# Kernel tuning notes

Measured on AMD Instinct MI355X. Metric: run time of the kernel, lower is better.

Reference implementation:

```python
import jax, jax.numpy as jnp
import numpy as np

B, W, D = 8, 1024, 1024
HEADS, KDIM, VDIM = 16, 64, 64


def setup_inputs() -> dict:
    key = jax.random.key(0)
    k1, k2, k3, k4 = jax.random.split(key, 4)
    # he_normal-ish scaling for weights
    s = (2.0 / D) ** 0.5
    return {
        "inputs": jax.random.normal(k1, (B, W, D), dtype=jnp.float32),
        "Wq": jax.random.normal(k2, (D, HEADS * KDIM), dtype=jnp.float32) * s,
        "Wk": jax.random.normal(k3, (D, HEADS * KDIM), dtype=jnp.float32) * s,
        "Wv": jax.random.normal(k4, (D, HEADS * VDIM), dtype=jnp.float32) * s,
    }


def reference(inputs, Wq, Wk, Wv):
    # Self-attention: memory = inputs
    bsz, win, _ = inputs.shape
    # DenseHeads: linear projection, reshaped to (B, W, heads, head_units)
    q = (inputs @ Wq).reshape(bsz, win, HEADS, KDIM)
    k = (inputs @ Wk).reshape(bsz, win, HEADS, KDIM)
    v = (inputs @ Wv).reshape(bsz, win, HEADS, VDIM)
    scale = KDIM ** (-0.5)
    # scores[b,q,h,m] = sum_k Q[b,q,h,k] * K[b,m,h,k]
    scores = jnp.einsum("bqhk,bmhk->bqhm", q, k) * scale
    attn = jax.nn.softmax(scores, axis=-1)
    # out[b,q,h,v] = sum_m attn[b,q,h,m] * V[b,m,h,v]
    out = jnp.einsum("bqhm,bmhv->bqhv", attn, v)
    return out
```

## Files before the change

### kernel.cpp

```cpp
#include <hip/hip_runtime.h>
#include <stdint.h>


using bf16x8 = __attribute__((ext_vector_type(8))) __bf16;
using f32x4  = __attribute__((ext_vector_type(4))) float;
using f16x4  = __attribute__((ext_vector_type(4))) _Float16;

union frag_u  { uint4 u4; bf16x8 f; };
union vfrag_u { uint2 u2; f16x4 f; };
union pfrag_u { unsigned int u[2]; f16x4 f; };

__device__ inline unsigned short f2bf(float x){
  unsigned int u = __float_as_uint(x);
  u += 0x7fffu + ((u >> 16) & 1u);
  return (unsigned short)(u >> 16);
}

__device__ inline unsigned int pkrtz_u32(float a, float b){
  auto r = __builtin_amdgcn_cvt_pkrtz(a, b);
  unsigned int u; __builtin_memcpy(&u, &r, 4); return u;
}

__device__ inline void gl_lds16(const void* g, void* l){
  __builtin_amdgcn_global_load_lds(
      (const __attribute__((address_space(1))) void*)g,
      (__attribute__((address_space(3))) void*)l, 16, 0, 0);
}

#define SBAR() do{ asm volatile("" ::: "memory"); __builtin_amdgcn_s_barrier(); asm volatile("" ::: "memory"); }while(0)
#define VMC(n)  asm volatile("s_waitcnt vmcnt(" #n ")" ::: "memory")

__global__ void cast_all(const float* __restrict__ X,
                         const float* __restrict__ Wq, const float* __restrict__ Wk,
                         const float* __restrict__ Wv,
                         unsigned short* __restrict__ Xb,
                         unsigned short* __restrict__ Wt){
  __shared__ float tile[64][65];
  int bid = blockIdx.x;
  if (bid < 8192){
    int i = (bid * 256 + threadIdx.x) * 4;
    float4 v = *(const float4*)(X + i);
    ushort4 o;
    o.x = f2bf(v.x); o.y = f2bf(v.y); o.z = f2bf(v.z); o.w = f2bf(v.w);
    *(ushort4*)(Xb + i) = o;
    return;
  }
  int id = bid - 8192;
  int proj = id >> 8;
  int rem  = id & 255;
  int kt = rem & 15, nt = rem >> 4;
  const float* Wsrc = (proj == 0) ? Wq : ((proj == 1) ? Wk : Wv);
  int k0 = kt * 64, n0 = nt * 64;
  int tx = threadIdx.x & 63, ty = threadIdx.x >> 6;
  for (int i = 0; i < 16; i++){
    int k = i * 4 + ty;
    tile[k][tx] = Wsrc[(k0 + k) * 1024 + n0 + tx];
  }
  __syncthreads();
  for (int i = 0; i < 16; i++){
    int n = i * 4 + ty;
    Wt[(proj * 1024 + n0 + n) * 1024 + k0 + tx] = f2bf(tile[tx][n]);
  }
}

__global__ __launch_bounds__(512, 2) void gemm_qkv(
    const unsigned short* __restrict__ Xb,
    const unsigned short* __restrict__ Wt,
    unsigned short* __restrict__ QK,
    unsigned short* __restrict__ Vt){
  __shared__ __align__(16) char Abuf[2][32768];
  __shared__ __align__(16) char Bbuf[2][24576];

  int bid = blockIdx.x;
  int tau = (bid & 7) * 64 + (bid >> 3);
  int by = tau >> 4, bx = tau & 15;
  int tid = threadIdx.x;
  int w = tid >> 6, lane = tid & 63;
  int li = lane & 15, g = lane >> 4;
  int lrow = lane >> 3;
  int wr = w >> 2, wc = w & 3;

  int xcol = ((lane & 7) ^ lrow) << 3;
  int aoff[4], boff[3];
#pragma unroll
  for (int j = 0; j < 4; j++)
    aoff[j] = (by * 256 + (j * 8 + w) * 8 + lrow) * 1024 + xcol;
#pragma unroll
  for (int j = 0; j < 3; j++)
    boff[j] = (bx * 192 + (j * 8 + w) * 8 + lrow) * 1024 + xcol;

  int swz  = (li & 7) << 4;
  int colA0 = (g * 16) ^ swz;
  int colA1 = (64 + g * 16) ^ swz;
  int aBase = (wr * 128 + li) * 128;
  int bBase = (wc * 48 + li) * 128;

  f32x4 acc[8][3] = {};
  frag_u bfr[3][2], a0[2][2], a1[2][2];

#define STA(buf, j, tt) gl_lds16(Xb + aoff[j] + (tt) * 64, &Abuf[buf][((j) * 8 + w) * 1024])
#define STB(buf, j, tt) gl_lds16(Wt + boff[j] + (tt) * 64, &Bbuf[buf][((j) * 8 + w) * 1024])
#define LDA(S, buf, m0) do{ \
  S[0][0].u4 = *(const uint4*)&Abuf[buf][aBase + (m0)     * 2048 + colA0]; \
  S[0][1].u4 = *(const uint4*)&Abuf[buf][aBase + (m0)     * 2048 + colA1]; \
  S[1][0].u4 = *(const uint4*)&Abuf[buf][aBase + (m0 + 1) * 2048 + colA0]; \
  S[1][1].u4 = *(const uint4*)&Abuf[buf][aBase + (m0 + 1) * 2048 + colA1]; }while(0)
#define LDB(buf) do{ \
  _Pragma("unroll") for (int n = 0; n < 3; n++){ \
    bfr[n][0].u4 = *(const uint4*)&Bbuf[buf][bBase + n * 2048 + colA0]; \
    bfr[n][1].u4 = *(const uint4*)&Bbuf[buf][bBase + n * 2048 + colA1]; } }while(0)
#define MFMAP(S, P) do{ __builtin_amdgcn_s_setprio(1); \
  _Pragma("unroll") for (int kk = 0; kk < 2; kk++) \
  _Pragma("unroll") for (int i = 0; i < 2; i++) \
  _Pragma("unroll") for (int n = 0; n < 3; n++) \
    acc[(P) * 2 + i][n] = __builtin_amdgcn_mfma_f32_16x16x32_bf16( \
        S[i][kk].f, bfr[n][kk].f, acc[(P) * 2 + i][n], 0, 0, 0); \
  __builtin_amdgcn_s_setprio(0); }while(0)

  STB(0, 0, 0); STB(0, 1, 0); STB(0, 2, 0);
  STA(0, 0, 0); STA(0, 1, 0); STA(0, 2, 0); STA(0, 3, 0);
  STB(1, 0, 1); STB(1, 1, 1); STB(1, 2, 1);
  VMC(3);
  SBAR();

  for (int t = 0; t < 16; ++t){
    int cur = t & 1, nxt = cur ^ 1;
    LDB(cur); LDA(a0, cur, 0);
    LDA(a1, cur, 2);
    if (t < 15){ STA(nxt, 0, t + 1); STA(nxt, 1, t + 1); }
    SBAR();
    MFMAP(a0, 0);
    SBAR();
    LDA(a0, cur, 4);
    if (t < 15){ STA(nxt, 2, t + 1); STA(nxt, 3, t + 1); }
    SBAR();
    MFMAP(a1, 1);
    SBAR();
    LDA(a1, cur, 6);
    if (t < 14){ STB(cur, 0, t + 2); STB(cur, 1, t + 2); }
    SBAR();
    MFMAP(a0, 2);
    SBAR();
    if (t < 14) STB(cur, 2, t + 2);
    SBAR();
    MFMAP(a1, 3);
    if (t < 14) { VMC(3); }
    else if (t == 14) { VMC(0); }
    SBAR();
  }
#undef STA
#undef STB
#undef LDA
#undef LDB
#undef MFMAP

  int row0 = by * 256 + wr * 128 + g * 4;
  int bb16 = (by >> 2) * 16;
#pragma unroll
  for (int n = 0; n < 3; n++){
    int cb = bx * 192 + wc * 48 + n * 16;
    if (cb < 2048){
      float sc = (cb < 1024) ? 0.1803368801111f : 1.0f;
#pragma unroll
      for (int m = 0; m < 8; m++){
        int row = row0 + m * 16;
#pragma unroll
        for (int r = 0; r < 4; r++)
          QK[(size_t)(row + r) * 2048 + cb + li] = f2bf(acc[m][n][r] * sc);
      }
    } else {
      int vc = cb + li - 2048;
      int hh = vc >> 6, dd = vc & 63;
#pragma unroll
      for (int m = 0; m < 8; m++){
        int mtok = (row0 + m * 16) & 1023;
        uint2 cv;
        cv.x = pkrtz_u32(acc[m][n][0], acc[m][n][1]);
        cv.y = pkrtz_u32(acc[m][n][2], acc[m][n][3]);
        *(uint2*)(Vt + ((size_t)(bb16 + hh) * 64 + dd) * 1024 + mtok) = cv;
      }
    }
  }
}

__global__ __launch_bounds__(256, 4) void attn(const unsigned short* __restrict__ QK,
                                               const unsigned short* __restrict__ Vt,
                                               float* __restrict__ Out){
  __shared__ __align__(16) unsigned short Kbuf[64 * 64];
  __shared__ __align__(16) unsigned short Vbuf[64 * 64];
  int id = blockIdx.x;
  int bh = id & 127, qb = id >> 7;
  int b = bh >> 4, h = bh & 15;
  int w = threadIdx.x >> 6, lane = threadIdx.x & 63;
  int g = lane >> 4, li = lane & 15;
  int lrow = lane >> 3, lcol = lane & 7;
  int scol = ((lcol ^ lrow) & 7) * 8;

  frag_u qf[2];
  {
    int tok = b * 1024 + qb * 64 + w * 16 + li;
    const unsigned short* qp = QK + (size_t)tok * 2048 + h * 64 + g * 8;
    qf[0].u4 = *(const uint4*)(qp);
    qf[1].u4 = *(const uint4*)(qp + 32);
  }

  f32x4 o[4] = {};
  f32x4 osum = {};
  const f32x4 bias = {-10.f, -10.f, -10.f, -10.f};
  pfrag_u ones;
  ones.u[0] = 0x3c003c00u; ones.u[1] = 0x3c003c00u;

  const unsigned short* Kg = QK + (size_t)b * 1024 * 2048 + 1024 + h * 64;
  const unsigned short* Vg = Vt + (size_t)bh * 65536;

  for (int mt = 0; mt < 16; mt++){
    int m0 = mt * 64;
    __syncthreads();
    for (int i = 0; i < 2; i++){
      int idx = w * 2 + i;
      int row = idx * 8 + lrow;
      gl_lds16(Kg + (size_t)(m0 + row) * 2048 + scol, Kbuf + idx * 512);
      gl_lds16(Vg + row * 1024 + m0 + scol,           Vbuf + idx * 512);
    }
    __syncthreads();

    f32x4 s[4];
    for (int t = 0; t < 4; t++) s[t] = bias;
    for (int t = 0; t < 4; t++){
      for (int c = 0; c < 2; c++){
        frag_u kf;
        kf.u4 = *(const uint4*)(Kbuf + (t * 16 + li) * 64 + ((((c << 2) + g) ^ (li & 7)) << 3));
        s[t] = __builtin_amdgcn_mfma_f32_16x16x32_bf16(kf.f, qf[c].f, s[t], 0, 0, 0);
      }
    }

    pfrag_u pf[4];
    for (int t = 0; t < 4; t++){
      float p0 = __builtin_exp2f(s[t][0]);
      float p1 = __builtin_exp2f(s[t][1]);
      float p2 = __builtin_exp2f(s[t][2]);
      float p3 = __builtin_exp2f(s[t][3]);
      pf[t].u[0] = pkrtz_u32(p0, p1);
      pf[t].u[1] = pkrtz_u32(p2, p3);
    }

    for (int t = 0; t < 4; t++)
      osum = __builtin_amdgcn_mfma_f32_16x16x16f16(ones.f, pf[t].f, osum, 0, 0, 0);
    for (int tv = 0; tv < 4; tv++){
      for (int t = 0; t < 4; t++){
        int gg = ((t * 2 + (g >> 1)) ^ (li & 7));
        vfrag_u vf;
        vf.u2 = *(const uint2*)(Vbuf + (tv * 16 + li) * 64 + gg * 8 + (g & 1) * 4);
        o[tv] = __builtin_amdgcn_mfma_f32_16x16x16f16(vf.f, pf[t].f, o[tv], 0, 0, 0);
      }
    }
  }

  float inv = 1.f / osum[0];

  int tok = b * 1024 + qb * 64 + w * 16 + li;
  float* op = Out + (size_t)tok * 1024 + h * 64 + g * 4;
  for (int tv = 0; tv < 4; tv++){
    float4 v4;
    v4.x = o[tv][0] * inv; v4.y = o[tv][1] * inv;
    v4.z = o[tv][2] * inv; v4.w = o[tv][3] * inv;
    *(float4*)(op + tv * 16) = v4;
  }
}

extern "C" void kernel_launch(void* const* d_in, const int* in_sizes, int n_in,
                              void* d_out, int out_size, void* d_ws, size_t ws_size,
                              hipStream_t stream) {
  const float* X  = (const float*)d_in[0];
  const float* Wq = (const float*)d_in[1];
  const float* Wk = (const float*)d_in[2];
  const float* Wv = (const float*)d_in[3];
  float* Out = (float*)d_out;
  char* ws = (char*)d_ws;
  unsigned short* Xb = (unsigned short*)(ws);
  unsigned short* Wt = (unsigned short*)(ws + (size_t)16 * 1024 * 1024);
  unsigned short* QK = (unsigned short*)(ws + (size_t)22 * 1024 * 1024);
  unsigned short* Vt = (unsigned short*)(ws + (size_t)54 * 1024 * 1024);

  cast_all<<<8960, 256, 0, stream>>>(X, Wq, Wk, Wv, Xb, Wt);
  gemm_qkv<<<512, 512, 0, stream>>>(Xb, Wt, QK, Vt);
  attn    <<<2048, 256, 0, stream>>>(QK, Vt, Out);
}
```

Measured before the change: 214.1 us.

## Split QKV GEMM tile across 16 waves with fewer accumulators per wave

Doubles the gemm_qkv block to 1024 threads (16 waves), so each wave computes a 64x48 sub-tile instead of 128x48. This halves the accumulator registers per wave and cuts the number of barriers per k-step. The global-to-LDS loads are redistributed so 8 waves issue two B loads and the rest issue one. More waves per block add latency hiding, but the larger workgroup brings heavier barrier synchronisation and less register headroom per wave.

```diff
diff --git a/kernel.cpp b/kernel.cpp
--- a/kernel.cpp
+++ b/kernel.cpp
@@ -63,7 +63,7 @@
   }
 }
 
-__global__ __launch_bounds__(512, 2) void gemm_qkv(
+__global__ __launch_bounds__(1024, 4) void gemm_qkv(
     const unsigned short* __restrict__ Xb,
     const unsigned short* __restrict__ Wt,
     unsigned short* __restrict__ QK,
@@ -79,82 +79,83 @@
   int li = lane & 15, g = lane >> 4;
   int lrow = lane >> 3;
   int wr = w >> 2, wc = w & 3;
+  int wu = __builtin_amdgcn_readfirstlane(w);
 
   int xcol = ((lane & 7) ^ lrow) << 3;
-  int aoff[4], boff[3];
-#pragma unroll
-  for (int j = 0; j < 4; j++)
-    aoff[j] = (by * 256 + (j * 8 + w) * 8 + lrow) * 1024 + xcol;
-#pragma unroll
-  for (int j = 0; j < 3; j++)
-    boff[j] = (bx * 192 + (j * 8 + w) * 8 + lrow) * 1024 + xcol;
+  int aoff0 = (by * 256 + w * 8 + lrow) * 1024 + xcol;
+  int aoff1 = (by * 256 + (16 + w) * 8 + lrow) * 1024 + xcol;
+  int bseg0 = (w < 8) ? w : (w + 8);
+  int bseg1 = w + 8;
+  int boff0 = (bx * 192 + bseg0 * 8 + lrow) * 1024 + xcol;
+  int boff1 = (bx * 192 + bseg1 * 8 + lrow) * 1024 + xcol;
 
   int swz  = (li & 7) << 4;
   int colA0 = (g * 16) ^ swz;
   int colA1 = (64 + g * 16) ^ swz;
-  int aBase = (wr * 128 + li) * 128;
+  int aBase = (wr * 64 + li) * 128;
   int bBase = (wc * 48 + li) * 128;
 
-  f32x4 acc[8][3] = {};
-  frag_u bfr[3][2], a0[2][2], a1[2][2];
-
-#define STA(buf, j, tt) gl_lds16(Xb + aoff[j] + (tt) * 64, &Abuf[buf][((j) * 8 + w) * 1024])
-#define STB(buf, j, tt) gl_lds16(Wt + boff[j] + (tt) * 64, &Bbuf[buf][((j) * 8 + w) * 1024])
-#define LDA(S, buf, m0) do{ \
-  S[0][0].u4 = *(const uint4*)&Abuf[buf][aBase + (m0)     * 2048 + colA0]; \
-  S[0][1].u4 = *(const uint4*)&Abuf[buf][aBase + (m0)     * 2048 + colA1]; \
-  S[1][0].u4 = *(const uint4*)&Abuf[buf][aBase + (m0 + 1) * 2048 + colA0]; \
-  S[1][1].u4 = *(const uint4*)&Abuf[buf][aBase + (m0 + 1) * 2048 + colA1]; }while(0)
+  f32x4 acc[4][3] = {};
+  frag_u bfr[3][2], af[2][2];
+
 #define LDB(buf) do{ \
   _Pragma("unroll") for (int n = 0; n < 3; n++){ \
     bfr[n][0].u4 = *(const uint4*)&Bbuf[buf][bBase + n * 2048 + colA0]; \
     bfr[n][1].u4 = *(const uint4*)&Bbuf[buf][bBase + n * 2048 + colA1]; } }while(0)
-#define MFMAP(S, P) do{ __builtin_amdgcn_s_setprio(1); \
+#define LDA2(buf, m0) do{ \
+  af[0][0].u4 = *(const uint4*)&Abuf[buf][aBase + (m0)     * 2048 + colA0]; \
+  af[0][1].u4 = *(const uint4*)&Abuf[buf][aBase + (m0)     * 2048 + colA1]; \
+  af[1][0].u4 = *(const uint4*)&Abuf[buf][aBase + (m0 + 1) * 2048 + colA0]; \
+  af[1][1].u4 = *(const uint4*)&Abuf[buf][aBase + (m0 + 1) * 2048 + colA1]; }while(0)
+#define MFMA6(P) do{ __builtin_amdgcn_s_setprio(1); \
   _Pragma("unroll") for (int kk = 0; kk < 2; kk++) \
   _Pragma("unroll") for (int i = 0; i < 2; i++) \
   _Pragma("unroll") for (int n = 0; n < 3; n++) \
-    acc[(P) * 2 + i][n] = __builtin_amdgcn_mfma_f32_16x16x32_bf16( \
-        S[i][kk].f, bfr[n][kk].f, acc[(P) * 2 + i][n], 0, 0, 0); \
+    acc[(P) + i][n] = __builtin_amdgcn_mfma_f32_16x16x32_bf16( \
+        af[i][kk].f, bfr[n][kk].f, acc[(P) + i][n], 0, 0, 0); \
   __builtin_amdgcn_s_setprio(0); }while(0)
 
-  STB(0, 0, 0); STB(0, 1, 0); STB(0, 2, 0);
-  STA(0, 0, 0); STA(0, 1, 0); STA(0, 2, 0); STA(0, 3, 0);
-  STB(1, 0, 1); STB(1, 1, 1); STB(1, 2, 1);
-  VMC(3);
+  gl_lds16(Wt + boff0, &Bbuf[0][bseg0 * 1024]);
+  if (wu < 8) gl_lds16(Wt + boff1, &Bbuf[0][bseg1 * 1024]);
+  gl_lds16(Xb + aoff0, &Abuf[0][w * 1024]);
+  gl_lds16(Xb + aoff1, &Abuf[0][(16 + w) * 1024]);
+  gl_lds16(Wt + boff0 + 64, &Bbuf[1][bseg0 * 1024]);
+  if (wu < 8){
+    gl_lds16(Wt + boff1 + 64, &Bbuf[1][bseg1 * 1024]);
+    VMC(2);
+  } else {
+    VMC(1);
+  }
   SBAR();
 
   for (int t = 0; t < 16; ++t){
     int cur = t & 1, nxt = cur ^ 1;
-    LDB(cur); LDA(a0, cur, 0);
-    LDA(a1, cur, 2);
-    if (t < 15){ STA(nxt, 0, t + 1); STA(nxt, 1, t + 1); }
+    LDB(cur);
+    LDA2(cur, 0);
+    if (t < 15){
+      gl_lds16(Xb + aoff0 + (t + 1) * 64, &Abuf[nxt][w * 1024]);
+      gl_lds16(Xb + aoff1 + (t + 1) * 64, &Abuf[nxt][(16 + w) * 1024]);
+    }
+    MFMA6(0);
     SBAR();
-    MFMAP(a0, 0);
+    LDA2(cur, 2);
+    if (t < 14){
+      gl_lds16(Wt + boff0 + (t + 2) * 64, &Bbuf[cur][bseg0 * 1024]);
+      if (wu < 8) gl_lds16(Wt + boff1 + (t + 2) * 64, &Bbuf[cur][bseg1 * 1024]);
+    }
+    MFMA6(2);
+    if (t < 14){
+      if (wu < 8) { VMC(2); } else { VMC(1); }
+    } else if (t == 14) {
+      VMC(0);
+    }
     SBAR();
-    LDA(a0, cur, 4);
-    if (t < 15){ STA(nxt, 2, t + 1); STA(nxt, 3, t + 1); }
-    SBAR();
-    MFMAP(a1, 1);
-    SBAR();
-    LDA(a1, cur, 6);
-    if (t < 14){ STB(cur, 0, t + 2); STB(cur, 1, t + 2); }
-    SBAR();
-    MFMAP(a0, 2);
-    SBAR();
-    if (t < 14) STB(cur, 2, t + 2);
-    SBAR();
-    MFMAP(a1, 3);
-    if (t < 14) { VMC(3); }
-    else if (t == 14) { VMC(0); }
-    SBAR();
-  }
-#undef STA
-#undef STB
-#undef LDA
+  }
 #undef LDB
-#undef MFMAP
-
-  int row0 = by * 256 + wr * 128 + g * 4;
+#undef LDA2
+#undef MFMA6
+
+  int row0 = by * 256 + wr * 64 + g * 4;
   int bb16 = (by >> 2) * 16;
 #pragma unroll
   for (int n = 0; n < 3; n++){
@@ -162,7 +163,7 @@
     if (cb < 2048){
       float sc = (cb < 1024) ? 0.1803368801111f : 1.0f;
 #pragma unroll
-      for (int m = 0; m < 8; m++){
+      for (int m = 0; m < 4; m++){
         int row = row0 + m * 16;
 #pragma unroll
         for (int r = 0; r < 4; r++)
@@ -172,7 +173,7 @@
       int vc = cb + li - 2048;
       int hh = vc >> 6, dd = vc & 63;
 #pragma unroll
-      for (int m = 0; m < 8; m++){
+      for (int m = 0; m < 4; m++){
         int mtok = (row0 + m * 16) & 1023;
         uint2 cv;
         cv.x = pkrtz_u32(acc[m][n][0], acc[m][n][1]);
@@ -283,6 +284,6 @@
   unsigned short* Vt = (unsigned short*)(ws + (size_t)54 * 1024 * 1024);
 
   cast_all<<<8960, 256, 0, stream>>>(X, Wq, Wk, Wv, Xb, Wt);
-  gemm_qkv<<<512, 512, 0, stream>>>(Xb, Wt, QK, Vt);
+  gemm_qkv<<<512, 1024, 0, stream>>>(Xb, Wt, QK, Vt);
   attn    <<<2048, 256, 0, stream>>>(QK, Vt, Out);
 }
```

Result: faster. 208.1 us (-2.8%).
